# Kernel optimization log

Hardware: AMD Instinct MI355X
Metric: run time of the kernel (lower is better)

## Reference

```python
import jax, jax.numpy as jnp
import numpy as np

B, S, DM1, DM2, DK, DV = 8, 2048, 768, 768, 64, 64
EPS = 1e-5


def setup_inputs() -> dict:
    key = jax.random.key(0)
    ks = jax.random.split(key, 8)
    s1 = 1.0 / np.sqrt(DM1)
    s2 = 1.0 / np.sqrt(DM2)
    return {
        "x_1": jax.random.normal(ks[0], (B, S, DM1), jnp.float32),
        "x_2": jax.random.normal(ks[1], (B, S, DM2), jnp.float32),
        "Wq": jax.random.uniform(ks[2], (DM1, DK), jnp.float32, -s1, s1),
        "bq": jnp.zeros((DK,), jnp.float32),
        "Wk": jax.random.uniform(ks[3], (DM2, DK), jnp.float32, -s2, s2),
        "bk": jnp.zeros((DK,), jnp.float32),
        "Wv": jax.random.uniform(ks[4], (DM2, DV), jnp.float32, -s2, s2),
        "bv": jnp.zeros((DV,), jnp.float32),
        "gamma": jnp.ones((DV,), jnp.float32),
        "beta": jnp.zeros((DV,), jnp.float32),
    }


def reference(x_1, x_2, Wq, bq, Wk, bk, Wv, bv, gamma, beta):
    q = jnp.einsum("bsd,dk->bsk", x_1, Wq) + bq            # [B,S,DK]
    k = jnp.einsum("bsd,dk->bsk", x_2, Wk) + bk            # [B,S,DK]
    v = jnp.einsum("bsd,dv->bsv", x_2, Wv) + bv            # [B,S,DV]
    scores = jnp.einsum("bqk,bsk->bqs", q, k) / jnp.sqrt(jnp.float32(DK))
    w = jax.nn.softmax(scores, axis=-1)                    # [B,S,S]
    # reverse-weight transform (reverse=True)
    dim = w.shape[1]
    w = (1.0 - w) / (dim - 1)
    attn = jnp.einsum("bqs,bsv->bqv", w, v)                # [B,S,DV]
    mu = jnp.mean(attn, axis=-1, keepdims=True)
    var = jnp.var(attn, axis=-1, keepdims=True)
    out = (attn - mu) * jax.lax.rsqrt(var + EPS) * gamma + beta
    return out
```

## Files before the change

kernel.cpp:

```cpp
#include <hip/hip_runtime.h>
#include <hip/hip_bf16.h>

#define BATCH 8
#define SEQ   2048
#define DM    768
#define DD    64
#define NSPLIT 4
#define SPLIT_S (SEQ / NSPLIT)
#define BS (BATCH * SEQ)

typedef __bf16 bf16x8 __attribute__((ext_vector_type(8)));
typedef float  f32x4  __attribute__((ext_vector_type(4)));
typedef short  short8 __attribute__((ext_vector_type(8)));
typedef short  short4v __attribute__((ext_vector_type(4)));

#define MFMA16(a, b, c) __builtin_amdgcn_mfma_f32_16x16x32_bf16((a), (b), (c), 0, 0, 0)

__device__ __forceinline__ short f2bf(float x) {
    unsigned u = __builtin_bit_cast(unsigned, x);
    u = (u + 0x7fffu + ((u >> 16) & 1u)) >> 16;
    return (short)u;
}
__device__ __forceinline__ float bf2f(short s) {
    unsigned u = ((unsigned)(unsigned short)s) << 16;
    return __builtin_bit_cast(float, u);
}

__global__ void prep_w_kernel(const float* __restrict__ Wq, const float* __restrict__ Wk,
                              const float* __restrict__ Wv, short* __restrict__ Wt) {
    int idx = blockIdx.x * 256 + threadIdx.x;
    if (idx >= 3 * DM * DD) return;
    int m = idx / (DM * DD);
    int r = (idx % (DM * DD)) / DD;
    int c = idx % DD;
    const float* W = (m == 0) ? Wq : (m == 1) ? Wk : Wv;
    float scale = (m == 0) ? 0.125f : 1.0f;
    Wt[m * DM * DD + c * DM + r] = f2bf(W[r * DD + c] * scale);
}

__global__ __launch_bounds__(64, 4) void proj_kernel(
        const float* __restrict__ x1, const float* __restrict__ x2,
        const short* __restrict__ Wt,
        const float* __restrict__ bq, const float* __restrict__ bk,
        const float* __restrict__ bv,
        short* __restrict__ Qs, short* __restrict__ Kb, short* __restrict__ Vtb,
        float* __restrict__ C) {
    const int lane = threadIdx.x, quad = lane >> 4, l15 = lane & 15;
    const int m  = blockIdx.x >> 10;
    const int r0 = (blockIdx.x & 1023) * 16;

    const float* xp = ((m == 0) ? x1 : x2) + (size_t)(r0 + l15) * DM + quad * 8;
    const short* wp = Wt + (size_t)m * DM * DD + (size_t)l15 * DM + quad * 8;

    f32x4 acc[4] = {};
    float4 ca = *(const float4*)xp;
    float4 cb = *(const float4*)(xp + 4);
    bf16x8 w0 = *(const bf16x8*)(wp);
    bf16x8 w1 = *(const bf16x8*)(wp + 16 * DM);
    bf16x8 w2 = *(const bf16x8*)(wp + 32 * DM);
    bf16x8 w3 = *(const bf16x8*)(wp + 48 * DM);
#pragma unroll
    for (int k0 = 0; k0 < DM; k0 += 32) {
        float4 na, nb; bf16x8 n0, n1, n2, n3;
        if (k0 + 32 < DM) {
            na = *(const float4*)(xp + k0 + 32);
            nb = *(const float4*)(xp + k0 + 36);
            n0 = *(const bf16x8*)(wp + k0 + 32);
            n1 = *(const bf16x8*)(wp + 16 * DM + k0 + 32);
            n2 = *(const bf16x8*)(wp + 32 * DM + k0 + 32);
            n3 = *(const bf16x8*)(wp + 48 * DM + k0 + 32);
        }
        bf16x8 af;
        af[0] = (__bf16)ca.x; af[1] = (__bf16)ca.y; af[2] = (__bf16)ca.z; af[3] = (__bf16)ca.w;
        af[4] = (__bf16)cb.x; af[5] = (__bf16)cb.y; af[6] = (__bf16)cb.z; af[7] = (__bf16)cb.w;
        acc[0] = MFMA16(af, w0, acc[0]);
        acc[1] = MFMA16(af, w1, acc[1]);
        acc[2] = MFMA16(af, w2, acc[2]);
        acc[3] = MFMA16(af, w3, acc[3]);
        ca = na; cb = nb; w0 = n0; w1 = n1; w2 = n2; w3 = n3;
    }

    if (m == 0) {
#pragma unroll
        for (int tn = 0; tn < 4; tn++) {
            int v = tn * 16 + l15;
            float bb = bq[v] * 0.125f;
#pragma unroll
            for (int r = 0; r < 4; r++)
                Qs[(size_t)(r0 + quad * 4 + r) * DD + v] = f2bf(acc[tn][r] + bb);
        }
    } else if (m == 1) {
#pragma unroll
        for (int tn = 0; tn < 4; tn++) {
            int v = tn * 16 + l15;
            float bb = bk[v];
#pragma unroll
            for (int r = 0; r < 4; r++)
                Kb[(size_t)(r0 + quad * 4 + r) * DD + v] = f2bf(acc[tn][r] + bb);
        }
    } else {
        const int b = r0 / SEQ;
        const int sbase = (r0 % SEQ) + quad * 4;
#pragma unroll
        for (int tn = 0; tn < 4; tn++) {
            int v = tn * 16 + l15;
            float bb = bv[v];
            short4v pk;
            float cs = 0.f;
#pragma unroll
            for (int r = 0; r < 4; r++) {
                pk[r] = f2bf(acc[tn][r] + bb);
                cs += bf2f(pk[r]);
            }
            *(short4v*)(Vtb + ((size_t)b * DD + v) * SEQ + sbase) = pk;
            cs += __shfl_xor(cs, 16);
            cs += __shfl_xor(cs, 32);
            if (quad == 0) atomicAdd(&C[b * DD + v], cs);
        }
    }
}

#define KSTR 80
#define PSTR 72
__global__ __launch_bounds__(256) void flash_kernel(
        const short* __restrict__ Q, const short* __restrict__ K,
        const short* __restrict__ Vt,
        short* __restrict__ Yp, float* __restrict__ Dp) {
    __shared__ __align__(16) short kl[64 * KSTR];
    __shared__ __align__(16) short vl[64 * KSTR];
    __shared__ __align__(16) short pb[4][16 * PSTR];
    const int tid  = threadIdx.x;
    const int wave = tid >> 6, lane = tid & 63, quad = lane >> 4, l15 = lane & 15;
    const int b = blockIdx.y, q0 = blockIdx.x * 64, split = blockIdx.z;

    const short* Qp = Q + ((size_t)(b * SEQ + q0) + wave * 16 + l15) * DD;
    bf16x8 qb0 = *(const bf16x8*)(Qp + quad * 8);
    bf16x8 qb1 = *(const bf16x8*)(Qp + 32 + quad * 8);

    const short* Kb = K  + (size_t)b * SEQ * DD;
    const short* Vb = Vt + (size_t)b * DD * SEQ;
    f32x4 y[4] = {};
    float den = 0.f;
    const int trow = tid >> 2, tcb = (tid & 3) * 2;
    short* pw = &pb[wave][0];

    const int send = split * SPLIT_S + SPLIT_S;
    for (int s0 = split * SPLIT_S; s0 < send; s0 += 64) {
        __syncthreads();
        const short* kp = Kb + (size_t)(s0 + trow) * DD + tcb * 8;
        *(short8*)&kl[trow * KSTR + tcb * 8]     = *(const short8*)kp;
        *(short8*)&kl[trow * KSTR + tcb * 8 + 8] = *(const short8*)(kp + 8);
        const short* vp = Vb + (size_t)trow * SEQ + s0 + tcb * 8;
        *(short8*)&vl[trow * KSTR + tcb * 8]     = *(const short8*)vp;
        *(short8*)&vl[trow * KSTR + tcb * 8 + 8] = *(const short8*)(vp + 8);
        __syncthreads();
#pragma unroll
        for (int tn = 0; tn < 4; tn++) {
            bf16x8 ka0 = *(const bf16x8*)&kl[(tn * 16 + l15) * KSTR + quad * 8];
            bf16x8 ka1 = *(const bf16x8*)&kl[(tn * 16 + l15) * KSTR + 32 + quad * 8];
            f32x4 z = {0.f, 0.f, 0.f, 0.f};
            z = MFMA16(ka0, qb0, z);
            z = MFMA16(ka1, qb1, z);
            short4v pk;
#pragma unroll
            for (int r = 0; r < 4; r++) {
                float p = __expf(z[r]);
                den += p;
                pk[r] = f2bf(p);
            }
            *(short4v*)&pw[l15 * PSTR + tn * 16 + quad * 4] = pk;
        }
#pragma unroll
        for (int kc = 0; kc < 2; kc++) {
            bf16x8 pB = *(const bf16x8*)&pw[l15 * PSTR + kc * 32 + quad * 8];
#pragma unroll
            for (int tn = 0; tn < 4; tn++) {
                bf16x8 va = *(const bf16x8*)&vl[(tn * 16 + l15) * KSTR + kc * 32 + quad * 8];
                y[tn] = MFMA16(va, pB, y[tn]);
            }
        }
    }
    den += __shfl_xor(den, 16);
    den += __shfl_xor(den, 32);
    const int qrow = b * SEQ + q0 + wave * 16 + l15;
    size_t ybase = (size_t)split * BS * DD + (size_t)qrow * DD;
#pragma unroll
    for (int tn = 0; tn < 4; tn++) {
        short4v pk;
#pragma unroll
        for (int r = 0; r < 4; r++) pk[r] = f2bf(y[tn][r]);
        *(short4v*)(Yp + ybase + tn * 16 + quad * 4) = pk;
    }
    if (quad == 0) Dp[split * BS + qrow] = den;
}

__global__ __launch_bounds__(256) void reduce_ln_kernel(
        const short* __restrict__ Yp, const float* __restrict__ Dp,
        const float* __restrict__ C, const float* __restrict__ gamma,
        const float* __restrict__ beta, float* __restrict__ out) {
    const int row = blockIdx.x * 4 + (threadIdx.x >> 6);
    const int v = threadIdx.x & 63;
    const int b = row >> 11;
    float Y = 0.f, D = 0.f;
#pragma unroll
    for (int s = 0; s < NSPLIT; s++) {
        Y += bf2f(Yp[((size_t)s * BS + row) * DD + v]);
        D += Dp[s * BS + row];
    }
    float attn = (C[b * DD + v] - Y / D) * (1.0f / (float)(SEQ - 1));
    float msum = attn, ssum = attn * attn;
#pragma unroll
    for (int m = 1; m < 64; m <<= 1) {
        msum += __shfl_xor(msum, m);
        ssum += __shfl_xor(ssum, m);
    }
    float mu = msum * (1.0f / 64.0f);
    float var = ssum * (1.0f / 64.0f) - mu * mu;
    float rs = rsqrtf(var + 1e-5f);
    out[(size_t)row * DD + v] = (attn - mu) * rs * gamma[v] + beta[v];
}

extern "C" void kernel_launch(void* const* d_in, const int* in_sizes, int n_in,
                              void* d_out, int out_size, void* d_ws, size_t ws_size,
                              hipStream_t stream) {
    const float* x1    = (const float*)d_in[0];
    const float* x2    = (const float*)d_in[1];
    const float* Wq    = (const float*)d_in[2];
    const float* bq    = (const float*)d_in[3];
    const float* Wk    = (const float*)d_in[4];
    const float* bk    = (const float*)d_in[5];
    const float* Wv    = (const float*)d_in[6];
    const float* bv    = (const float*)d_in[7];
    const float* gamma = (const float*)d_in[8];
    const float* beta  = (const float*)d_in[9];
    float* out = (float*)d_out;

    char* ws = (char*)d_ws;
    short* Qs  = (short*)(ws);
    short* Kb  = (short*)(ws + (2ull << 20));
    short* Vtb = (short*)(ws + (4ull << 20));
    short* Wt  = (short*)(ws + (6ull << 20));
    float* Cc  = (float*)(ws + (6ull << 20) + 3 * DM * DD * 2);
    short* Yp  = (short*)(ws + (7ull << 20));
    float* Dp  = (float*)(ws + (16ull << 20));

    hipMemsetAsync(Cc, 0, BATCH * DD * sizeof(float), stream);
    prep_w_kernel<<<576, 256, 0, stream>>>(Wq, Wk, Wv, Wt);
    proj_kernel<<<3072, 64, 0, stream>>>(x1, x2, Wt, bq, bk, bv, Qs, Kb, Vtb, Cc);
    flash_kernel<<<dim3(32, 8, NSPLIT), 256, 0, stream>>>(Qs, Kb, Vtb, Yp, Dp);
    reduce_ln_kernel<<<BS / 4, 256, 0, stream>>>(Yp, Dp, Cc, gamma, beta, out);
}
```

Measured before the change: 199.5 us.

## Fuse K/V projections sharing x_2 and read K/V directly from global in flash

```diff
diff --git a/kernel.cpp b/kernel.cpp
--- a/kernel.cpp
+++ b/kernel.cpp
@@ -24,6 +24,12 @@
 __device__ __forceinline__ float bf2f(short s) {
     unsigned u = ((unsigned)(unsigned short)s) << 16;
     return __builtin_bit_cast(float, u);
+}
+__device__ __forceinline__ bf16x8 cvt8(float4 a, float4 b) {
+    bf16x8 r;
+    r[0] = (__bf16)a.x; r[1] = (__bf16)a.y; r[2] = (__bf16)a.z; r[3] = (__bf16)a.w;
+    r[4] = (__bf16)b.x; r[5] = (__bf16)b.y; r[6] = (__bf16)b.z; r[7] = (__bf16)b.w;
+    return r;
 }
 
 __global__ void prep_w_kernel(const float* __restrict__ Wq, const float* __restrict__ Wk,
@@ -38,7 +44,7 @@
     Wt[m * DM * DD + c * DM + r] = f2bf(W[r * DD + c] * scale);
 }
 
-__global__ __launch_bounds__(64, 4) void proj_kernel(
+__global__ __launch_bounds__(64) void proj_kernel(
         const float* __restrict__ x1, const float* __restrict__ x2,
         const short* __restrict__ Wt,
         const float* __restrict__ bq, const float* __restrict__ bk,
@@ -50,55 +56,73 @@
     const int r0 = (blockIdx.x & 1023) * 16;
 
     const float* xp = ((m == 0) ? x1 : x2) + (size_t)(r0 + l15) * DM + quad * 8;
-    const short* wp = Wt + (size_t)m * DM * DD + (size_t)l15 * DM + quad * 8;
-
-    f32x4 acc[4] = {};
-    float4 ca = *(const float4*)xp;
-    float4 cb = *(const float4*)(xp + 4);
-    bf16x8 w0 = *(const bf16x8*)(wp);
-    bf16x8 w1 = *(const bf16x8*)(wp + 16 * DM);
-    bf16x8 w2 = *(const bf16x8*)(wp + 32 * DM);
-    bf16x8 w3 = *(const bf16x8*)(wp + 48 * DM);
-#pragma unroll
-    for (int k0 = 0; k0 < DM; k0 += 32) {
-        float4 na, nb; bf16x8 n0, n1, n2, n3;
-        if (k0 + 32 < DM) {
-            na = *(const float4*)(xp + k0 + 32);
-            nb = *(const float4*)(xp + k0 + 36);
-            n0 = *(const bf16x8*)(wp + k0 + 32);
-            n1 = *(const bf16x8*)(wp + 16 * DM + k0 + 32);
-            n2 = *(const bf16x8*)(wp + 32 * DM + k0 + 32);
-            n3 = *(const bf16x8*)(wp + 48 * DM + k0 + 32);
-        }
-        bf16x8 af;
-        af[0] = (__bf16)ca.x; af[1] = (__bf16)ca.y; af[2] = (__bf16)ca.z; af[3] = (__bf16)ca.w;
-        af[4] = (__bf16)cb.x; af[5] = (__bf16)cb.y; af[6] = (__bf16)cb.z; af[7] = (__bf16)cb.w;
-        acc[0] = MFMA16(af, w0, acc[0]);
-        acc[1] = MFMA16(af, w1, acc[1]);
-        acc[2] = MFMA16(af, w2, acc[2]);
-        acc[3] = MFMA16(af, w3, acc[3]);
-        ca = na; cb = nb; w0 = n0; w1 = n1; w2 = n2; w3 = n3;
-    }
+    const short* wpa = Wt + (size_t)m * DM * DD + (size_t)l15 * DM + quad * 8;
+    const short* wpv = Wt + 2 * (size_t)DM * DD + (size_t)l15 * DM + quad * 8;
+
+    f32x4 acc0[4] = {}, acc1[4] = {};
+    float4 xa0 = *(const float4*)xp;
+    float4 xb0 = *(const float4*)(xp + 4);
+    float4 xa1 = *(const float4*)(xp + 32);
+    float4 xb1 = *(const float4*)(xp + 36);
 
     if (m == 0) {
+#pragma unroll
+        for (int k0 = 0; k0 < DM; k0 += 64) {
+            const int kp1 = (k0 + 64 < DM) ? k0 + 64 : DM - 32;
+            const int kp2 = (k0 + 96 < DM) ? k0 + 96 : DM - 32;
+            float4 na0 = *(const float4*)(xp + kp1);
+            float4 nb0 = *(const float4*)(xp + kp1 + 4);
+            float4 na1 = *(const float4*)(xp + kp2);
+            float4 nb1 = *(const float4*)(xp + kp2 + 4);
+            bf16x8 af = cvt8(xa0, xb0);
+#pragma unroll
+            for (int tn = 0; tn < 4; tn++)
+                acc0[tn] = MFMA16(af, *(const bf16x8*)(wpa + (size_t)tn * 16 * DM + k0), acc0[tn]);
+            af = cvt8(xa1, xb1);
+#pragma unroll
+            for (int tn = 0; tn < 4; tn++)
+                acc0[tn] = MFMA16(af, *(const bf16x8*)(wpa + (size_t)tn * 16 * DM + k0 + 32), acc0[tn]);
+            xa0 = na0; xb0 = nb0; xa1 = na1; xb1 = nb1;
+        }
 #pragma unroll
         for (int tn = 0; tn < 4; tn++) {
             int v = tn * 16 + l15;
             float bb = bq[v] * 0.125f;
 #pragma unroll
             for (int r = 0; r < 4; r++)
-                Qs[(size_t)(r0 + quad * 4 + r) * DD + v] = f2bf(acc[tn][r] + bb);
-        }
-    } else if (m == 1) {
+                Qs[(size_t)(r0 + quad * 4 + r) * DD + v] = f2bf(acc0[tn][r] + bb);
+        }
+    } else {
+#pragma unroll
+        for (int k0 = 0; k0 < DM; k0 += 64) {
+            const int kp1 = (k0 + 64 < DM) ? k0 + 64 : DM - 32;
+            const int kp2 = (k0 + 96 < DM) ? k0 + 96 : DM - 32;
+            float4 na0 = *(const float4*)(xp + kp1);
+            float4 nb0 = *(const float4*)(xp + kp1 + 4);
+            float4 na1 = *(const float4*)(xp + kp2);
+            float4 nb1 = *(const float4*)(xp + kp2 + 4);
+            bf16x8 af = cvt8(xa0, xb0);
+#pragma unroll
+            for (int tn = 0; tn < 4; tn++) {
+                acc0[tn] = MFMA16(af, *(const bf16x8*)(wpa + (size_t)tn * 16 * DM + k0), acc0[tn]);
+                acc1[tn] = MFMA16(af, *(const bf16x8*)(wpv + (size_t)tn * 16 * DM + k0), acc1[tn]);
+            }
+            af = cvt8(xa1, xb1);
+#pragma unroll
+            for (int tn = 0; tn < 4; tn++) {
+                acc0[tn] = MFMA16(af, *(const bf16x8*)(wpa + (size_t)tn * 16 * DM + k0 + 32), acc0[tn]);
+                acc1[tn] = MFMA16(af, *(const bf16x8*)(wpv + (size_t)tn * 16 * DM + k0 + 32), acc1[tn]);
+            }
+            xa0 = na0; xb0 = nb0; xa1 = na1; xb1 = nb1;
+        }
 #pragma unroll
         for (int tn = 0; tn < 4; tn++) {
             int v = tn * 16 + l15;
             float bb = bk[v];
 #pragma unroll
             for (int r = 0; r < 4; r++)
-                Kb[(size_t)(r0 + quad * 4 + r) * DD + v] = f2bf(acc[tn][r] + bb);
-        }
-    } else {
+                Kb[(size_t)(r0 + quad * 4 + r) * DD + v] = f2bf(acc0[tn][r] + bb);
+        }
         const int b = r0 / SEQ;
         const int sbase = (r0 % SEQ) + quad * 4;
 #pragma unroll
@@ -109,7 +133,7 @@
             float cs = 0.f;
 #pragma unroll
             for (int r = 0; r < 4; r++) {
-                pk[r] = f2bf(acc[tn][r] + bb);
+                pk[r] = f2bf(acc1[tn][r] + bb);
                 cs += bf2f(pk[r]);
             }
             *(short4v*)(Vtb + ((size_t)b * DD + v) * SEQ + sbase) = pk;
@@ -120,14 +144,11 @@
     }
 }
 
-#define KSTR 80
-#define PSTR 72
+#define PSTR 88
 __global__ __launch_bounds__(256) void flash_kernel(
         const short* __restrict__ Q, const short* __restrict__ K,
         const short* __restrict__ Vt,
         short* __restrict__ Yp, float* __restrict__ Dp) {
-    __shared__ __align__(16) short kl[64 * KSTR];
-    __shared__ __align__(16) short vl[64 * KSTR];
     __shared__ __align__(16) short pb[4][16 * PSTR];
     const int tid  = threadIdx.x;
     const int wave = tid >> 6, lane = tid & 63, quad = lane >> 4, l15 = lane & 15;
@@ -137,27 +158,19 @@
     bf16x8 qb0 = *(const bf16x8*)(Qp + quad * 8);
     bf16x8 qb1 = *(const bf16x8*)(Qp + 32 + quad * 8);
 
-    const short* Kb = K  + (size_t)b * SEQ * DD;
-    const short* Vb = Vt + (size_t)b * DD * SEQ;
+    const short* Kp = K  + (size_t)b * SEQ * DD + (size_t)l15 * DD + quad * 8;
+    const short* Vp = Vt + (size_t)b * DD * SEQ + (size_t)l15 * SEQ + quad * 8;
     f32x4 y[4] = {};
     float den = 0.f;
-    const int trow = tid >> 2, tcb = (tid & 3) * 2;
     short* pw = &pb[wave][0];
 
     const int send = split * SPLIT_S + SPLIT_S;
     for (int s0 = split * SPLIT_S; s0 < send; s0 += 64) {
-        __syncthreads();
-        const short* kp = Kb + (size_t)(s0 + trow) * DD + tcb * 8;
-        *(short8*)&kl[trow * KSTR + tcb * 8]     = *(const short8*)kp;
-        *(short8*)&kl[trow * KSTR + tcb * 8 + 8] = *(const short8*)(kp + 8);
-        const short* vp = Vb + (size_t)trow * SEQ + s0 + tcb * 8;
-        *(short8*)&vl[trow * KSTR + tcb * 8]     = *(const short8*)vp;
-        *(short8*)&vl[trow * KSTR + tcb * 8 + 8] = *(const short8*)(vp + 8);
-        __syncthreads();
-#pragma unroll
-        for (int tn = 0; tn < 4; tn++) {
-            bf16x8 ka0 = *(const bf16x8*)&kl[(tn * 16 + l15) * KSTR + quad * 8];
-            bf16x8 ka1 = *(const bf16x8*)&kl[(tn * 16 + l15) * KSTR + 32 + quad * 8];
+#pragma unroll
+        for (int tn = 0; tn < 4; tn++) {
+            const short* kf = Kp + (size_t)(s0 + tn * 16) * DD;
+            bf16x8 ka0 = *(const bf16x8*)(kf);
+            bf16x8 ka1 = *(const bf16x8*)(kf + 32);
             f32x4 z = {0.f, 0.f, 0.f, 0.f};
             z = MFMA16(ka0, qb0, z);
             z = MFMA16(ka1, qb1, z);
@@ -175,7 +188,7 @@
             bf16x8 pB = *(const bf16x8*)&pw[l15 * PSTR + kc * 32 + quad * 8];
 #pragma unroll
             for (int tn = 0; tn < 4; tn++) {
-                bf16x8 va = *(const bf16x8*)&vl[(tn * 16 + l15) * KSTR + kc * 32 + quad * 8];
+                bf16x8 va = *(const bf16x8*)(Vp + (size_t)(tn * 16) * SEQ + s0 + kc * 32);
                 y[tn] = MFMA16(va, pB, y[tn]);
             }
         }
@@ -237,7 +250,7 @@
 
     char* ws = (char*)d_ws;
     short* Qs  = (short*)(ws);
-    short* Kb  = (short*)(ws + (2ull << 20));
+    short* Kbf = (short*)(ws + (2ull << 20));
     short* Vtb = (short*)(ws + (4ull << 20));
     short* Wt  = (short*)(ws + (6ull << 20));
     float* Cc  = (float*)(ws + (6ull << 20) + 3 * DM * DD * 2);
@@ -246,7 +259,7 @@
 
     hipMemsetAsync(Cc, 0, BATCH * DD * sizeof(float), stream);
     prep_w_kernel<<<576, 256, 0, stream>>>(Wq, Wk, Wv, Wt);
-    proj_kernel<<<3072, 64, 0, stream>>>(x1, x2, Wt, bq, bk, bv, Qs, Kb, Vtb, Cc);
-    flash_kernel<<<dim3(32, 8, NSPLIT), 256, 0, stream>>>(Qs, Kb, Vtb, Yp, Dp);
+    proj_kernel<<<2048, 64, 0, stream>>>(x1, x2, Wt, bq, bk, bv, Qs, Kbf, Vtb, Cc);
+    flash_kernel<<<dim3(32, 8, NSPLIT), 256, 0, stream>>>(Qs, Kbf, Vtb, Yp, Dp);
     reduce_ln_kernel<<<BS / 4, 256, 0, stream>>>(Yp, Dp, Cc, gamma, beta, out);
 }
```

Result: slower. 240.2 us (+20.4%).
